# Kernel optimization log

Measured on AMD Instinct MI355X. Metric: run time of the kernel, lower is better.

Reference implementation:

```python
import jax, jax.numpy as jnp
import numpy as np
from jax import lax

B, N, C = 4, 16384, 128
HEADS = 2
SR = 4
EPS = 1e-6


def setup_inputs() -> dict:
    key = jax.random.key(0)
    ks = jax.random.split(key, 6)
    s = 0.02
    return {
        "x": jax.random.normal(ks[0], (B, N, C), jnp.float32),
        "Wq": jax.random.normal(ks[1], (C, C), jnp.float32) * s,
        "Wk": jax.random.normal(ks[2], (C, C), jnp.float32) * s,
        "Wv": jax.random.normal(ks[3], (C, C), jnp.float32) * s,
        "Wproj": jax.random.normal(ks[4], (C, C), jnp.float32) * s,
        "sr_kernel": jax.random.normal(ks[5], (SR, SR, C, C), jnp.float32) * s,
        "sr_bias": jnp.zeros((C,), jnp.float32),
        "gamma": jnp.ones((C,), jnp.float32),
        "beta": jnp.zeros((C,), jnp.float32),
    }


def reference(x, Wq, Wk, Wv, Wproj, sr_kernel, sr_bias, gamma, beta):
    b, n, c = x.shape
    h = w = int(np.sqrt(n))          # H = W = sqrt(N), static
    dh = c // HEADS                  # head dim
    scale = dh ** -0.5

    # Q projection -> (B, heads, N, dh)
    q = (x @ Wq).reshape(b, n, HEADS, dh).transpose(0, 2, 1, 3)

    # Spatial reduction of K/V: conv stride=SR, 'same' padding, then LayerNorm
    x_img = x.reshape(b, h, w, c)
    x_ = lax.conv_general_dilated(
        x_img, sr_kernel, window_strides=(SR, SR), padding="SAME",
        dimension_numbers=("NHWC", "HWIO", "NHWC"))
    x_ = x_ + sr_bias
    x_ = x_.reshape(b, -1, c)        # (B, N', C), N' = (H/SR)*(W/SR)
    mu = jnp.mean(x_, axis=-1, keepdims=True)
    var = jnp.mean(jnp.square(x_ - mu), axis=-1, keepdims=True)
    x_ = (x_ - mu) * lax.rsqrt(var + EPS) * gamma + beta

    k = (x_ @ Wk).reshape(b, -1, HEADS, dh).transpose(0, 2, 1, 3)  # (B,h,N',dh)
    v = (x_ @ Wv).reshape(b, -1, HEADS, dh).transpose(0, 2, 1, 3)

    attn = jnp.einsum("bhqd,bhkd->bhqk", q, k) * scale
    attn = jax.nn.softmax(attn, axis=-1)
    out = jnp.einsum("bhqk,bhkd->bhqd", attn, v)
    out = out.transpose(0, 2, 1, 3).reshape(b, n, c)
    return out @ Wproj
```

## Files before the change

kernel.cpp:

```cpp
#include <hip/hip_runtime.h>
#include <hip/hip_bf16.h>

typedef unsigned short u16;
typedef __attribute__((ext_vector_type(8))) short short8;
typedef __attribute__((ext_vector_type(4))) float f32x4;
typedef __attribute__((ext_vector_type(2))) float f32x2;
typedef __attribute__((ext_vector_type(16))) float f32x16;

#define MFMA16(a, b, c) __builtin_amdgcn_mfma_f32_16x16x32_bf16((a), (b), (c), 0, 0, 0)
#define MFMA32(a, b, c) __builtin_amdgcn_mfma_f32_32x32x16_bf16((a), (b), (c), 0, 0, 0)

__device__ __forceinline__ u16 f2bf(float f) {
  __hip_bfloat16 h = __float2bfloat16(f);
  u16 r;
  __builtin_memcpy(&r, &h, 2);
  return r;
}
__device__ __forceinline__ float bf2f(u16 h) {
  unsigned u = ((unsigned)h) << 16;
  float f;
  __builtin_memcpy(&f, &u, 4);
  return f;
}
__device__ __forceinline__ unsigned pk2(float a, float b) {
  unsigned r;
  asm("v_cvt_pk_bf16_f32 %0, %1, %2" : "=v"(r) : "v"(a), "v"(b));
  return r;
}
__device__ __forceinline__ short8 ld8(const void* src, int idx, int isf32) {
  short8 v;
  if (isf32) {
    const float4* s = (const float4*)((const float*)src + idx);
    float4 p0 = s[0], p1 = s[1];
    unsigned d0 = pk2(p0.x, p0.y), d1 = pk2(p0.z, p0.w);
    unsigned d2 = pk2(p1.x, p1.y), d3 = pk2(p1.z, p1.w);
    uint4 dd = {d0, d1, d2, d3};
    __builtin_memcpy(&v, &dd, 16);
  } else {
    v = *(const short8*)((const u16*)src + idx);
  }
  return v;
}
__device__ __forceinline__ float ld1(const void* src, int idx, int isf32) {
  return isf32 ? ((const float*)src)[idx] : bf2f(((const u16*)src)[idx]);
}
__device__ __forceinline__ int detect_isf32(const u16* xw) {
  int lane = threadIdx.x & 63;
  int cnt = 0;
#pragma unroll
  for (int i = 0; i < 16; ++i) {
    u16 w = xw[lane * 16 + i];
    cnt += (((w >> 7) & 0xFF) >= 0xC0) ? 1 : 0;
  }
#pragma unroll
  for (int off = 1; off < 64; off <<= 1) cnt += __shfl_xor(cnt, off, 64);
  return cnt >= 32;
}

__global__ void prep_kernel(const void* __restrict__ srk, const void* __restrict__ Wq,
                            const void* __restrict__ Wk, const void* __restrict__ Wv,
                            const void* __restrict__ Wp, const void* __restrict__ x,
                            u16* __restrict__ WcT) {
  const int isf32 = detect_isf32((const u16*)x);
  int gid = blockIdx.x * 256 + threadIdx.x;
  if (gid >= 327680) return;
  int cout = (gid >> 7) & 127, cin = gid & 127;
  float v;
  if (gid < 262144) {
    int mat = gid >> 14;
    v = ld1(srk, mat * 16384 + cin * 128 + cout, isf32);
  } else {
    int mat = (gid - 262144) >> 14;
    const void* src = (mat == 0) ? Wq : (mat == 1) ? Wk : (mat == 2) ? Wv : Wp;
    v = ld1(src, cin * 128 + cout, isf32);
  }
  WcT[gid] = f2bf(v);
}

__launch_bounds__(1024, 4)
__global__ void conv_ln_kv_kernel(const void* __restrict__ x, const u16* __restrict__ wcT,
                                  const void* __restrict__ sr_bias,
                                  const void* __restrict__ gamma,
                                  const void* __restrict__ beta,
                                  const u16* __restrict__ WkT, const u16* __restrict__ WvT,
                                  u16* __restrict__ Kb, u16* __restrict__ Vt) {
  extern __shared__ char cws[];
  float* Racc = (float*)cws;
  u16* Xs = (u16*)(cws + 16 * 16 * 128 * 4);
  const int isf32 = detect_isf32((const u16*)x);
  const int tid = threadIdx.x;
  const int wave = tid >> 6, lane = tid & 63;
  const int quad = lane >> 4, l16 = lane & 15;
  const int g = blockIdx.x;

  const int row = g * 16 + l16;
  const int pb = row >> 10, rem = row & 1023, oh = rem >> 5, ow = rem & 31;
  const int xbase = ((pb * 128 + oh * 4) * 128 + ow * 4) * 128;

  f32x4 acc[8];
#pragma unroll
  for (int i = 0; i < 8; ++i) acc[i] = (f32x4){0.f, 0.f, 0.f, 0.f};

  {
    const int r = wave >> 2, sc = wave & 3;
    short8 a[4];
#pragma unroll
    for (int kc = 0; kc < 4; ++kc)
      a[kc] = ld8(x, xbase + r * 16384 + sc * 128 + kc * 32 + quad * 8, isf32);
#pragma unroll
    for (int nt = 0; nt < 8; ++nt)
#pragma unroll
      for (int kc = 0; kc < 4; ++kc) {
        short8 bw = *(const short8*)(wcT + wave * 16384 + (nt * 16 + l16) * 128 +
                                     kc * 32 + quad * 8);
        acc[nt] = MFMA16(a[kc], bw, acc[nt]);
      }
  }
#pragma unroll
  for (int nt = 0; nt < 8; ++nt)
#pragma unroll
    for (int rr = 0; rr < 4; ++rr)
      Racc[(wave * 16 + quad * 4 + rr) * 128 + nt * 16 + l16] = acc[nt][rr];
  __syncthreads();

  {
    const int lrow = wave, c0 = lane * 2;
    f32x2 rsum = (f32x2){0.f, 0.f};
#pragma unroll
    for (int w = 0; w < 16; ++w) {
      f32x2 t = *(const f32x2*)&Racc[(w * 16 + lrow) * 128 + c0];
      rsum[0] += t[0];
      rsum[1] += t[1];
    }
    float v0 = rsum[0] + ld1(sr_bias, c0, isf32);
    float v1 = rsum[1] + ld1(sr_bias, c0 + 1, isf32);
    float sum = v0 + v1, sum2 = v0 * v0 + v1 * v1;
#pragma unroll
    for (int off = 1; off < 64; off <<= 1) {
      sum += __shfl_xor(sum, off, 64);
      sum2 += __shfl_xor(sum2, off, 64);
    }
    const float mu = sum * (1.f / 128.f);
    const float var = sum2 * (1.f / 128.f) - mu * mu;
    const float rinv = rsqrtf(fmaxf(var, 0.f) + 1e-6f);
    float y0 = (v0 - mu) * rinv * ld1(gamma, c0, isf32) + ld1(beta, c0, isf32);
    float y1 = (v1 - mu) * rinv * ld1(gamma, c0 + 1, isf32) + ld1(beta, c0 + 1, isf32);
    *(unsigned*)&Xs[lrow * 136 + c0] = pk2(y0, y1);
  }
  __syncthreads();

  short8 a2[4];
#pragma unroll
  for (int kc = 0; kc < 4; ++kc)
    a2[kc] = *(const short8*)&Xs[l16 * 136 + kc * 32 + quad * 8];
  const u16* Wm = (wave & 1) ? WvT : WkT;
  const int nt = wave >> 1;
  f32x4 a3 = (f32x4){0.f, 0.f, 0.f, 0.f};
#pragma unroll
  for (int kc = 0; kc < 4; ++kc) {
    short8 bm = *(const short8*)(Wm + (nt * 16 + l16) * 128 + kc * 32 + quad * 8);
    a3 = MFMA16(a2[kc], bm, a3);
  }
#pragma unroll
  for (int rr = 0; rr < 4; ++rr) {
    const int rowg = g * 16 + quad * 4 + rr;
    const int b = rowg >> 10, key = rowg & 1023;
    const int c = nt * 16 + l16;
    if (wave & 1)
      Vt[(b * 128 + c) * 1024 + key] = f2bf(a3[rr]);
    else
      Kb[rowg * 128 + c] = f2bf(a3[rr]);
  }
}

__launch_bounds__(256, 2)
__global__ void attn_kernel(const void* __restrict__ x, const u16* __restrict__ WqT,
                            const u16* __restrict__ WpT, const u16* __restrict__ Kb,
                            const u16* __restrict__ Vt, float* __restrict__ out) {
  extern __shared__ u16 lds[];
  u16* Ks = lds;
  u16* Vs = Ks + 64 * 136;
  u16* Pp = Vs + 128 * 72;
  const int isf32 = detect_isf32((const u16*)x);
  const int tid = threadIdx.x;
  const int wave = tid >> 6, lane = tid & 63;
  const int quad = lane >> 4, l16 = lane & 15;
  const int q32 = lane & 31, hi = lane >> 5;
  const int swz = (blockIdx.x & 7) * 64 + (blockIdx.x >> 3);
  const int b = swz >> 7;
  const int row0 = (swz & 127) * 128;
  const int wrow = wave * 32;
  u16* Pw = Pp + wave * 2304;
  u16* Fw = lds + wave * 4352;

  const float qscale = 0.125f * 1.4426950408889634f;

#pragma unroll
  for (int mt = 0; mt < 2; ++mt) {
    short8 xb[4];
#pragma unroll
    for (int kc = 0; kc < 4; ++kc)
      xb[kc] = ld8(x, (b * 16384 + row0 + wrow + mt * 16 + l16) * 128 + kc * 32 + quad * 8,
                   isf32);
#pragma unroll
    for (int nt = 0; nt < 8; ++nt) {
      f32x4 qa = (f32x4){0.f, 0.f, 0.f, 0.f};
#pragma unroll
      for (int kc = 0; kc < 4; ++kc) {
        short8 w = *(const short8*)(WqT + (nt * 16 + l16) * 128 + kc * 32 + quad * 8);
        qa = MFMA16(w, xb[kc], qa);
      }
      uint2 pk = {pk2(qa[0] * qscale, qa[1] * qscale), pk2(qa[2] * qscale, qa[3] * qscale)};
      *(uint2*)&Fw[(mt * 16 + l16) * 136 + nt * 16 + quad * 4] = pk;
    }
  }
  short8 qf[2][4];
#pragma unroll
  for (int h = 0; h < 2; ++h)
#pragma unroll
    for (int s = 0; s < 4; ++s)
      qf[h][s] = *(const short8*)&Fw[q32 * 136 + h * 64 + s * 16 + hi * 8];

  f32x16 o[2][2];
#pragma unroll
  for (int h = 0; h < 2; ++h)
#pragma unroll
    for (int dt = 0; dt < 2; ++dt)
#pragma unroll
      for (int r = 0; r < 16; ++r) o[h][dt][r] = 0.f;
  float l[2] = {0.f, 0.f};

  const int kkey = tid >> 2, kseg = tid & 3;
  const int vc = tid >> 1, vseg = tid & 1;

  for (int ch = 0; ch < 16; ++ch) {
    __syncthreads();
    {
      const uint4* src = (const uint4*)(Kb + (b * 1024 + ch * 64 + kkey) * 128 + kseg * 32);
      uint4* dst = (uint4*)&Ks[kkey * 136 + kseg * 32];
      dst[0] = src[0];
      dst[1] = src[1];
      dst[2] = src[2];
      dst[3] = src[3];
    }
    {
      const uint4* src = (const uint4*)(Vt + (b * 128 + vc) * 1024 + ch * 64 + vseg * 32);
      uint4* dst = (uint4*)&Vs[vc * 72 + vseg * 32];
      dst[0] = src[0];
      dst[1] = src[1];
      dst[2] = src[2];
      dst[3] = src[3];
    }
    __syncthreads();
#pragma unroll
    for (int h = 0; h < 2; ++h) {
#pragma unroll
      for (int kt = 0; kt < 2; ++kt) {
        f32x16 S;
#pragma unroll
        for (int r = 0; r < 16; ++r) S[r] = 0.f;
#pragma unroll
        for (int s = 0; s < 4; ++s) {
          short8 kf = *(const short8*)&Ks[(kt * 32 + q32) * 136 + h * 64 + s * 16 + hi * 8];
          S = MFMA32(kf, qf[h][s], S);
        }
        float lh = 0.f;
#pragma unroll
        for (int rp = 0; rp < 8; ++rp) {
          float p0 = exp2f(S[2 * rp]), p1 = exp2f(S[2 * rp + 1]);
          lh += p0 + p1;
          *(unsigned*)&Pw[q32 * 72 + kt * 32 + (rp >> 1) * 8 + hi * 4 + (rp & 1) * 2] =
              pk2(p0, p1);
        }
        l[h] += lh;
      }
      short8 pf[4];
#pragma unroll
      for (int s = 0; s < 4; ++s)
        pf[s] = *(const short8*)&Pw[q32 * 72 + s * 16 + hi * 8];
      __builtin_amdgcn_s_setprio(1);
#pragma unroll
      for (int dt = 0; dt < 2; ++dt)
#pragma unroll
        for (int s = 0; s < 4; ++s) {
          short8 vf = *(const short8*)&Vs[(h * 64 + dt * 32 + q32) * 72 + s * 16 + hi * 8];
          o[h][dt] = MFMA32(vf, pf[s], o[h][dt]);
        }
      __builtin_amdgcn_s_setprio(0);
    }
  }

#pragma unroll
  for (int h = 0; h < 2; ++h) {
    float t = l[h];
    t += __shfl_xor(t, 32, 64);
    const float inv = 1.0f / t;
#pragma unroll
    for (int dt = 0; dt < 2; ++dt)
#pragma unroll
      for (int r = 0; r < 16; ++r) o[h][dt][r] *= inv;
  }

  __syncthreads();

#pragma unroll
  for (int h = 0; h < 2; ++h)
#pragma unroll
    for (int dt = 0; dt < 2; ++dt)
#pragma unroll
      for (int rp = 0; rp < 8; ++rp) {
        *(unsigned*)&Fw[q32 * 136 + h * 64 + dt * 32 + (rp >> 1) * 8 + hi * 4 +
                        (rp & 1) * 2] = pk2(o[h][dt][2 * rp], o[h][dt][2 * rp + 1]);
      }
#pragma unroll
  for (int mt = 0; mt < 2; ++mt) {
    short8 of[4];
#pragma unroll
    for (int kc = 0; kc < 4; ++kc)
      of[kc] = *(const short8*)&Fw[(mt * 16 + l16) * 136 + kc * 32 + quad * 8];
#pragma unroll
    for (int nt = 0; nt < 8; ++nt) {
      f32x4 pa = (f32x4){0.f, 0.f, 0.f, 0.f};
#pragma unroll
      for (int kc = 0; kc < 4; ++kc) {
        short8 w = *(const short8*)(WpT + (nt * 16 + l16) * 128 + kc * 32 + quad * 8);
        pa = MFMA16(of[kc], w, pa);
      }
#pragma unroll
      for (int rr = 0; rr < 4; ++rr)
        out[(b * 16384 + row0 + wrow + mt * 16 + quad * 4 + rr) * 128 + nt * 16 + l16] =
            pa[rr];
    }
  }
}

extern "C" void kernel_launch(void* const* d_in, const int* in_sizes, int n_in,
                              void* d_out, int out_size, void* d_ws, size_t ws_size,
                              hipStream_t stream) {
  (void)in_sizes; (void)n_in; (void)out_size; (void)ws_size;
  const void* x = d_in[0];
  const void* Wq = d_in[1];
  const void* Wk = d_in[2];
  const void* Wv = d_in[3];
  const void* Wp = d_in[4];
  const void* srk = d_in[5];
  const void* sbias = d_in[6];
  const void* gamma = d_in[7];
  const void* beta = d_in[8];
  float* out = (float*)d_out;
  u16* ws = (u16*)d_ws;

  u16* WcT = ws;
  u16* WqT = ws + 262144;
  u16* WkT = ws + 278528;
  u16* WvT = ws + 294912;
  u16* WpT = ws + 311296;
  u16* Kb = ws + 327680;
  u16* Vt = ws + 851968;

  prep_kernel<<<dim3(1280), dim3(256), 0, stream>>>(srk, Wq, Wk, Wv, Wp, x, WcT);
  conv_ln_kv_kernel<<<dim3(256), dim3(1024), 16 * 16 * 128 * 4 + 16 * 136 * 2, stream>>>(
      x, WcT, sbias, gamma, beta, WkT, WvT, Kb, Vt);
  attn_kernel<<<dim3(512), dim3(256), (64 * 136 + 128 * 72 + 4 * 2304) * 2, stream>>>(
      x, WqT, WpT, Kb, Vt, out);
}
```

Baseline: 209.5 us.

## Register-prefetch next K/V chunk in attention and coalesce prep/V stores

The attention kernel now loads the next K/V chunk from global memory into registers while the current chunk is computed, then writes those registers to LDS at the start of the next iteration. This hides global load latency behind the MFMA work. The prep kernel now reads the weights contiguously and scatters the writes instead. The conv/LN kernel packs four V values into one 8-byte store. The prefetch holds 32 extra VGPRs per thread, which may reduce occupancy or cause spills under the launch bounds of 256 threads and 2 blocks.

```diff
diff --git a/kernel.cpp b/kernel.cpp
--- a/kernel.cpp
+++ b/kernel.cpp
@@ -64,17 +64,20 @@
   const int isf32 = detect_isf32((const u16*)x);
   int gid = blockIdx.x * 256 + threadIdx.x;
   if (gid >= 327680) return;
-  int cout = (gid >> 7) & 127, cin = gid & 127;
   float v;
+  int dst;
   if (gid < 262144) {
-    int mat = gid >> 14;
-    v = ld1(srk, mat * 16384 + cin * 128 + cout, isf32);
+    int mat = gid >> 14, cin = (gid >> 7) & 127, cout = gid & 127;
+    v = ld1(srk, gid, isf32);
+    dst = mat * 16384 + cout * 128 + cin;
   } else {
-    int mat = (gid - 262144) >> 14;
+    int g2 = gid - 262144;
+    int mat = g2 >> 14, cin = (g2 >> 7) & 127, cout = g2 & 127;
     const void* src = (mat == 0) ? Wq : (mat == 1) ? Wk : (mat == 2) ? Wv : Wp;
     v = ld1(src, cin * 128 + cout, isf32);
-  }
-  WcT[gid] = f2bf(v);
+    dst = 262144 + mat * 16384 + cout * 128 + cin;
+  }
+  WcT[dst] = f2bf(v);
 }
 
 __launch_bounds__(1024, 4)
@@ -161,15 +164,15 @@
     short8 bm = *(const short8*)(Wm + (nt * 16 + l16) * 128 + kc * 32 + quad * 8);
     a3 = MFMA16(a2[kc], bm, a3);
   }
-#pragma unroll
-  for (int rr = 0; rr < 4; ++rr) {
-    const int rowg = g * 16 + quad * 4 + rr;
-    const int b = rowg >> 10, key = rowg & 1023;
-    const int c = nt * 16 + l16;
-    if (wave & 1)
-      Vt[(b * 128 + c) * 1024 + key] = f2bf(a3[rr]);
-    else
-      Kb[rowg * 128 + c] = f2bf(a3[rr]);
+  const int rowg0 = g * 16 + quad * 4;
+  const int b0 = rowg0 >> 10, key0 = rowg0 & 1023;
+  const int c = nt * 16 + l16;
+  if (wave & 1) {
+    uint2 pv = {pk2(a3[0], a3[1]), pk2(a3[2], a3[3])};
+    *(uint2*)&Vt[(b0 * 128 + c) * 1024 + key0] = pv;
+  } else {
+#pragma unroll
+    for (int rr = 0; rr < 4; ++rr) Kb[(rowg0 + rr) * 128 + c] = f2bf(a3[rr]);
   }
 }
 
@@ -195,6 +198,15 @@
 
   const float qscale = 0.125f * 1.4426950408889634f;
 
+  const int kkey = tid >> 2, kseg = tid & 3;
+  const int vc = tid >> 1, vseg = tid & 1;
+  const u16* ksrc = Kb + (b * 1024 + kkey) * 128 + kseg * 32;
+  const u16* vsrc = Vt + (b * 128 + vc) * 1024 + vseg * 32;
+  uint4 kr0 = ((const uint4*)ksrc)[0], kr1 = ((const uint4*)ksrc)[1],
+        kr2 = ((const uint4*)ksrc)[2], kr3 = ((const uint4*)ksrc)[3];
+  uint4 vr0 = ((const uint4*)vsrc)[0], vr1 = ((const uint4*)vsrc)[1],
+        vr2 = ((const uint4*)vsrc)[2], vr3 = ((const uint4*)vsrc)[3];
+
 #pragma unroll
   for (int mt = 0; mt < 2; ++mt) {
     short8 xb[4];
@@ -220,6 +232,7 @@
 #pragma unroll
     for (int s = 0; s < 4; ++s)
       qf[h][s] = *(const short8*)&Fw[q32 * 136 + h * 64 + s * 16 + hi * 8];
+  __syncthreads();
 
   f32x16 o[2][2];
 #pragma unroll
@@ -230,28 +243,22 @@
       for (int r = 0; r < 16; ++r) o[h][dt][r] = 0.f;
   float l[2] = {0.f, 0.f};
 
-  const int kkey = tid >> 2, kseg = tid & 3;
-  const int vc = tid >> 1, vseg = tid & 1;
-
   for (int ch = 0; ch < 16; ++ch) {
+    {
+      uint4* kd = (uint4*)&Ks[kkey * 136 + kseg * 32];
+      kd[0] = kr0; kd[1] = kr1; kd[2] = kr2; kd[3] = kr3;
+      uint4* vd = (uint4*)&Vs[vc * 72 + vseg * 32];
+      vd[0] = vr0; vd[1] = vr1; vd[2] = vr2; vd[3] = vr3;
+    }
     __syncthreads();
-    {
-      const uint4* src = (const uint4*)(Kb + (b * 1024 + ch * 64 + kkey) * 128 + kseg * 32);
-      uint4* dst = (uint4*)&Ks[kkey * 136 + kseg * 32];
-      dst[0] = src[0];
-      dst[1] = src[1];
-      dst[2] = src[2];
-      dst[3] = src[3];
-    }
-    {
-      const uint4* src = (const uint4*)(Vt + (b * 128 + vc) * 1024 + ch * 64 + vseg * 32);
-      uint4* dst = (uint4*)&Vs[vc * 72 + vseg * 32];
-      dst[0] = src[0];
-      dst[1] = src[1];
-      dst[2] = src[2];
-      dst[3] = src[3];
-    }
-    __syncthreads();
+    if (ch < 15) {
+      const u16* kn = ksrc + (ch + 1) * 8192;
+      kr0 = ((const uint4*)kn)[0]; kr1 = ((const uint4*)kn)[1];
+      kr2 = ((const uint4*)kn)[2]; kr3 = ((const uint4*)kn)[3];
+      const u16* vn = vsrc + (ch + 1) * 64;
+      vr0 = ((const uint4*)vn)[0]; vr1 = ((const uint4*)vn)[1];
+      vr2 = ((const uint4*)vn)[2]; vr3 = ((const uint4*)vn)[3];
+    }
 #pragma unroll
     for (int h = 0; h < 2; ++h) {
 #pragma unroll
@@ -288,6 +295,7 @@
         }
       __builtin_amdgcn_s_setprio(0);
     }
+    __syncthreads();
   }
 
 #pragma unroll
@@ -300,8 +308,6 @@
 #pragma unroll
       for (int r = 0; r < 16; ++r) o[h][dt][r] *= inv;
   }
-
-  __syncthreads();
 
 #pragma unroll
   for (int h = 0; h < 2; ++h)
```

Result: faster. 204.7 us (-2.3%).
